# Optimization experiments

Measured on AMD Instinct MI355X. Metric: run time of the kernel, lower is better.

The kernel has to match this reference:

```python
import jax, jax.numpy as jnp
import numpy as np

N_QUBITS = 8
N_CYCLES = 4
N_GATES = 10
MEAS_QUBITS = (3, 7)
BATCH = 16384


def _apply_ry_batched(state, angles, w):
    # angles: [B] per-example RY angle on wire w. state: [B,2,...,2]
    half = angles * 0.5
    c = jnp.cos(half).astype(jnp.complex64)
    s = jnp.sin(half).astype(jnp.complex64)
    U = jnp.stack([jnp.stack([c, -s], -1), jnp.stack([s, c], -1)], -2)  # [B,2,2]
    st = jnp.moveaxis(state, w + 1, -1)
    st = jnp.einsum('bij,b...j->b...i', U, st)
    return jnp.moveaxis(st, -1, w + 1)


def _apply_cnot(state, c, t):
    st = jnp.moveaxis(state, (c + 1, t + 1), (-2, -1))
    st = jnp.concatenate([st[..., 0:1, :], st[..., 1:2, ::-1]], axis=-2)
    return jnp.moveaxis(st, (-2, -1), (c + 1, t + 1))


def _apply_crx(state, theta, c, t):
    # CRX: RX(theta) on target when control=1 (torchquantum convention)
    half = theta * 0.5
    co = jnp.cos(half).astype(jnp.complex64)
    si = (-1j * jnp.sin(half)).astype(jnp.complex64)
    st = jnp.moveaxis(state, (c + 1, t + 1), (-2, -1))
    s1 = st[..., 1, :]
    s1 = jnp.stack([co * s1[..., 0] + si * s1[..., 1],
                    si * s1[..., 0] + co * s1[..., 1]], -1)
    st = jnp.concatenate([st[..., 0:1, :], s1[..., None, :]], axis=-2)
    return jnp.moveaxis(st, (-2, -1), (c + 1, t + 1))


def _expval_z(probs, w):
    axes = tuple(a for a in range(1, N_QUBITS + 1) if a != w + 1)
    m = jnp.sum(probs, axis=axes)  # [B,2]
    return m[:, 0] - m[:, 1]


def _forward(x, crx_theta, w1, b1, w2, b2):
    B = x.shape[0]
    state = jnp.zeros((B, 2 ** N_QUBITS), jnp.complex64).at[:, 0].set(1.0)
    state = state.reshape((B,) + (2,) * N_QUBITS)
    # encoding ansatz: per cycle, RY(x[:,cyc,q]) on each qubit + CNOT ring
    for cyc in range(N_CYCLES):
        for q in range(N_QUBITS):
            state = _apply_ry_batched(state, x[:, cyc, q], q)
        for q in range(N_QUBITS):
            state = _apply_cnot(state, q, (q + 1) % N_QUBITS)
    # trainable CRX layer
    for i in range(N_GATES):
        state = _apply_crx(state, crx_theta[i], i % N_QUBITS, (i + 1) % N_QUBITS)
    probs = jnp.abs(state) ** 2  # real, [B,2,...,2]
    feats = jnp.stack([_expval_z(probs, q) for q in MEAS_QUBITS], -1)  # [B,2]
    h = jnp.tanh(feats @ w1.T + b1)
    return jax.nn.sigmoid(h @ w2.T + b2)  # [B,1]


def setup_inputs() -> dict:
    key = jax.random.key(0)
    ks = jax.random.split(key, 6)
    x = jax.random.normal(ks[0], (BATCH, N_CYCLES, N_QUBITS), jnp.float32)
    crx_theta = jax.random.normal(ks[1], (N_GATES,), jnp.float32) * 0.1
    w1 = jax.random.normal(ks[2], (10, 2), jnp.float32) * (1.0 / np.sqrt(2.0))
    b1 = jnp.zeros((10,), jnp.float32)
    w2 = jax.random.normal(ks[3], (1, 10), jnp.float32) * (1.0 / np.sqrt(10.0))
    b2 = jnp.zeros((1,), jnp.float32)
    return {"x": x, "crx_theta": crx_theta, "w1": w1, "b1": b1, "w2": w2, "b2": b2}


def reference(x, crx_theta, w1, b1, w2, b2):
    return _forward(x, crx_theta, w1, b1, w2, b2)
```

## Files before the change

kernel.cpp:

```cpp
#include <hip/hip_runtime.h>
#include <math.h>


typedef _Float16 h2 __attribute__((ext_vector_type(2)));

#define H2I(v) __builtin_bit_cast(int, (v))
#define I2H(v) __builtin_bit_cast(h2, (v))
#define RLF(v, i) __int_as_float(__builtin_amdgcn_readlane(__float_as_int(v), (i)))
#define RLH(v, i) I2H(__builtin_amdgcn_readlane(H2I(v), (i)))
#define BPH(a, v) I2H(__builtin_amdgcn_ds_bpermute((a), H2I(v)))
#define BPFS(a, v) __int_as_float(__builtin_amdgcn_ds_bpermute((a), __float_as_int(v)))
#define DPPH(v, ctrl) I2H(__builtin_amdgcn_update_dpp(0, H2I(v), (ctrl), 0xf, 0xf, true))
#define DPPF(v, ctrl) __uint_as_float((unsigned)__builtin_amdgcn_update_dpp( \
    0, (int)__float_as_uint(v), (ctrl), 0xf, 0xf, true))
#define NEGH(v) I2H(H2I(v) ^ 0x80008000)
#define SELH(c, a, b) I2H((c) ? H2I(a) : H2I(b))
#define FMH(a, b, c) __builtin_elementwise_fma((a), (b), (c))
#define HONE  I2H(0x3C003C00)
#define HZERO I2H(0)

#define PX1H(v)  DPPH((v), 0xB1)
#define PX2H(v)  DPPH((v), 0x4E)
#define PX4H(v)  DPPH(DPPH((v), 0x141), 0x1B)
#define PX8H(v)  DPPH((v), 0x128)
#define BP16(v)  BPH(a16, (v))
#define BP32(v)  BPH(a32, (v))
#define PX1S(v)  DPPF((v), 0xB1)
#define PX2S(v)  DPPF((v), 0x4E)
#define PX4S(v)  DPPF(DPPF((v), 0x141), 0x1B)
#define PX8S(v)  DPPF((v), 0x128)

__device__ __forceinline__ h2 mkh(float a, float b) {
    h2 r; r.x = (_Float16)a; r.y = (_Float16)b; return r;
}

__global__ __launch_bounds__(256, 8) void vqcnn_wave(
    const float* __restrict__ x,
    const float* __restrict__ crx_theta,
    const float* __restrict__ w1,
    const float* __restrict__ b1,
    const float* __restrict__ w2,
    const float* __restrict__ b2,
    float* __restrict__ out)
{
    const int lane = threadIdx.x & 63;
    const int bA   = blockIdx.x * 8 + (threadIdx.x >> 6) * 2;
    const int bB   = bA + 1;

    float cvA, svA, cvB, svB;
    {
        float aA = 0.f, aB = 0.f;
        if (lane < 32)      { aA = x[bA * 32 + lane]; aB = x[bB * 32 + lane]; }
        else if (lane < 42) { aA = aB = crx_theta[lane - 32]; }
        __sincosf(0.5f * aA, &svA, &cvA);
        __sincosf(0.5f * aB, &svB, &cvB);
    }
    const h2 cvP = mkh(cvA, cvB);
    const h2 svP = mkh(svA, svB);

    const int a16 = (lane ^ 16) << 2;
    const int a32 = (lane ^ 32) << 2;
    const int g0  = lane ^ (lane >> 1);
    const int aE  = g0 << 2;
    const int aO  = (g0 ^ 32) << 2;
    const bool l0r = (lane & 1) != 0;

    h2 vv0, vv1, vv2, vv3;
    {
        float LA = (lane & 32) ? RLF(svA, 3) : RLF(cvA, 3);
        float LB = (lane & 32) ? RLF(svB, 3) : RLF(cvB, 3);
        LA *= (lane & 16) ? RLF(svA, 4) : RLF(cvA, 4);
        LB *= (lane & 16) ? RLF(svB, 4) : RLF(cvB, 4);
        LA *= (lane &  8) ? RLF(svA, 5) : RLF(cvA, 5);
        LB *= (lane &  8) ? RLF(svB, 5) : RLF(cvB, 5);
        LA *= (lane &  4) ? RLF(svA, 6) : RLF(cvA, 6);
        LB *= (lane &  4) ? RLF(svB, 6) : RLF(cvB, 6);
        LA *= (lane &  2) ? RLF(svA, 7) : RLF(cvA, 7);
        LB *= (lane &  2) ? RLF(svB, 7) : RLF(cvB, 7);
        LA *= (lane &  1) ? RLF(svA, 0) : RLF(cvA, 0);
        LB *= (lane &  1) ? RLF(svB, 0) : RLF(cvB, 0);
        const float c1A = RLF(cvA, 1), s1A = RLF(svA, 1);
        const float c2A = RLF(cvA, 2), s2A = RLF(svA, 2);
        const float c1B = RLF(cvB, 1), s1B = RLF(svB, 1);
        const float c2B = RLF(cvB, 2), s2B = RLF(svB, 2);
        vv0 = mkh(LA * c1A * c2A, LB * c1B * c2B);
        vv1 = mkh(LA * c1A * s2A, LB * c1B * s2B);
        vv2 = mkh(LA * s1A * c2A, LB * s1B * c2B);
        vv3 = mkh(LA * s1A * s2A, LB * s1B * s2B);
    }

#define RINGH() {                                                            \
    const h2 z0 = SELH(l0r, vv2, vv0);                                       \
    const h2 z1 = SELH(l0r, vv3, vv1);                                       \
    const h2 z2 = SELH(l0r, vv1, vv3);                                       \
    const h2 z3 = SELH(l0r, vv0, vv2);                                       \
    vv0 = BPH(aE, z0); vv1 = BPH(aO, z1);                                    \
    vv2 = BPH(aE, z2); vv3 = BPH(aO, z3); }
    RINGH()

#define RY_L(ia, mask, EX) {                                                 \
    const h2 c = RLH(cvP, (ia)), s = RLH(svP, (ia));                         \
    const h2 sn = SELH((lane & (mask)) != 0, s, NEGH(s));                    \
    const h2 p0 = EX(vv0), p1 = EX(vv1);                                     \
    const h2 p2 = EX(vv2), p3 = EX(vv3);                                     \
    vv0 = FMH(sn, p0, c * vv0); vv1 = FMH(sn, p1, c * vv1);                  \
    vv2 = FMH(sn, p2, c * vv2); vv3 = FMH(sn, p3, c * vv3); }

#define RY_S1(ia) {                                                          \
    const h2 c = RLH(cvP, (ia)), s = RLH(svP, (ia)), ns = NEGH(s);           \
    const h2 n0 = FMH(ns, vv2, c * vv0), n2 = FMH(s, vv0, c * vv2);          \
    const h2 n1 = FMH(ns, vv3, c * vv1), n3 = FMH(s, vv1, c * vv3);          \
    vv0 = n0; vv1 = n1; vv2 = n2; vv3 = n3; }

#define RY_S0(ia) {                                                          \
    const h2 c = RLH(cvP, (ia)), s = RLH(svP, (ia)), ns = NEGH(s);           \
    const h2 n0 = FMH(ns, vv1, c * vv0), n1 = FMH(s, vv0, c * vv1);          \
    const h2 n2 = FMH(ns, vv3, c * vv2), n3 = FMH(s, vv2, c * vv3);          \
    vv0 = n0; vv1 = n1; vv2 = n2; vv3 = n3; }

    #pragma unroll
    for (int cyc = 1; cyc < 4; ++cyc) {
        const int base = cyc * 8;
        RY_L(base + 0,  1, PX1H)
        RY_S1(base + 1)
        RY_S0(base + 2)
        RY_L(base + 3, 32, BP32)
        RY_L(base + 4, 16, BP16)
        RY_L(base + 5,  8, PX8H)
        RY_L(base + 6,  4, PX4H)
        RY_L(base + 7,  2, PX2H)
        RINGH()
    }

    h2 rr0 = vv0, rr1 = vv1, rr2 = vv2, rr3 = vv3;
    h2 ii0 = HZERO, ii1 = HZERO, ii2 = HZERO, ii3 = HZERO;

#define CRX_G(gi, cmask, EX) {                                               \
    const bool ct = (lane & (cmask)) != 0;                                   \
    const h2 c = SELH(ct, RLH(cvP, 32 + (gi)), HONE);                        \
    const h2 s = SELH(ct, RLH(svP, 32 + (gi)), HZERO);                       \
    const h2 ns = NEGH(s);                                                   \
    const h2 pr0 = EX(rr0), pi0 = EX(ii0);                                   \
    const h2 pr1 = EX(rr1), pi1 = EX(ii1);                                   \
    const h2 pr2 = EX(rr2), pi2 = EX(ii2);                                   \
    const h2 pr3 = EX(rr3), pi3 = EX(ii3);                                   \
    rr0 = FMH(s, pi0, c * rr0); ii0 = FMH(ns, pr0, c * ii0);                 \
    rr1 = FMH(s, pi1, c * rr1); ii1 = FMH(ns, pr1, c * ii1);                 \
    rr2 = FMH(s, pi2, c * rr2); ii2 = FMH(ns, pr2, c * ii2);                 \
    rr3 = FMH(s, pi3, c * rr3); ii3 = FMH(ns, pr3, c * ii3); }

#define CRX_SLOT1(gi) {                                                      \
    const bool ct = (lane & 1) != 0;                                         \
    const h2 c = SELH(ct, RLH(cvP, 32 + (gi)), HONE);                        \
    const h2 s = SELH(ct, RLH(svP, 32 + (gi)), HZERO);                       \
    const h2 ns = NEGH(s);                                                   \
    const h2 nr0 = FMH(s, ii2, c * rr0), ni0 = FMH(ns, rr2, c * ii0);        \
    const h2 nr2 = FMH(s, ii0, c * rr2), ni2 = FMH(ns, rr0, c * ii2);        \
    const h2 nr1 = FMH(s, ii3, c * rr1), ni1 = FMH(ns, rr3, c * ii1);        \
    const h2 nr3 = FMH(s, ii1, c * rr3), ni3 = FMH(ns, rr1, c * ii3);        \
    rr0 = nr0; ii0 = ni0; rr1 = nr1; ii1 = ni1;                              \
    rr2 = nr2; ii2 = ni2; rr3 = nr3; ii3 = ni3; }

#define CRX_SLOT0(gi) {                                                      \
    const h2 c = RLH(cvP, 32 + (gi)), s = RLH(svP, 32 + (gi)), ns = NEGH(s); \
    const h2 nr2 = FMH(s, ii3, c * rr2), ni2 = FMH(ns, rr3, c * ii2);        \
    const h2 nr3 = FMH(s, ii2, c * rr3), ni3 = FMH(ns, rr2, c * ii3);        \
    rr2 = nr2; ii2 = ni2; rr3 = nr3; ii3 = ni3; }

    CRX_SLOT1(0)
    CRX_SLOT0(1)
    {
        const h2 c = RLH(cvP, 34), s = RLH(svP, 34), ns = NEGH(s);
        const h2 pr1 = BP32(rr1), pi1 = BP32(ii1);
        const h2 pr3 = BP32(rr3), pi3 = BP32(ii3);
        rr1 = FMH(s, pi1, c * rr1); ii1 = FMH(ns, pr1, c * ii1);
        rr3 = FMH(s, pi3, c * rr3); ii3 = FMH(ns, pr3, c * ii3);
    }
    CRX_G(3, 32, BP16)
    CRX_G(4, 16, PX8H)
    CRX_G(5,  8, PX4H)
    CRX_G(6,  4, PX2H)
    CRX_G(7,  2, PX1H)
    CRX_SLOT1(8)
    CRX_SLOT0(9)

    const h2 pp0 = FMH(rr0, rr0, ii0 * ii0);
    const h2 pp1 = FMH(rr1, rr1, ii1 * ii1);
    const h2 pp2 = FMH(rr2, rr2, ii2 * ii2);
    const h2 pp3 = FMH(rr3, rr3, ii3 * ii3);
    const h2 ap  = (pp0 + pp1) + (pp2 + pp3);
    const float aA = (float)ap.x, aB = (float)ap.y;
    float z3A = (lane & 32) ? -aA : aA, z3B = (lane & 32) ? -aB : aB;
    float z7A = (lane &  2) ? -aA : aA, z7B = (lane &  2) ? -aB : aB;
    z3A += PX1S(z3A); z3B += PX1S(z3B); z7A += PX1S(z7A); z7B += PX1S(z7B);
    z3A += PX2S(z3A); z3B += PX2S(z3B); z7A += PX2S(z7A); z7B += PX2S(z7B);
    z3A += PX4S(z3A); z3B += PX4S(z3B); z7A += PX4S(z7A); z7B += PX4S(z7B);
    z3A += PX8S(z3A); z3B += PX8S(z3B); z7A += PX8S(z7A); z7B += PX8S(z7B);
    z3A += BPFS(a16, z3A); z3B += BPFS(a16, z3B);
    z7A += BPFS(a16, z7A); z7B += BPFS(a16, z7B);
    z3A += BPFS(a32, z3A); z3B += BPFS(a32, z3B);
    z7A += BPFS(a32, z7A); z7B += BPFS(a32, z7B);

    float wa = 0.f, wb = 0.f, bb = 0.f, wc = 0.f;
    if (lane < 10) {
        wa = w1[2 * lane];
        wb = w1[2 * lane + 1];
        bb = b1[lane];
        wc = w2[lane];
    }
    const float zA = fmaf(wa, z3A, fmaf(wb, z7A, bb));
    const float zB = fmaf(wa, z3B, fmaf(wb, z7B, bb));
    const float eA = __expf(2.0f * zA), eB = __expf(2.0f * zB);
    const float hA = 1.0f - 2.0f * __builtin_amdgcn_rcpf(eA + 1.0f);
    const float hB = 1.0f - 2.0f * __builtin_amdgcn_rcpf(eB + 1.0f);
    float accA = wc * hA, accB = wc * hB;
    accA += PX1S(accA); accB += PX1S(accB);
    accA += PX2S(accA); accB += PX2S(accB);
    accA += PX4S(accA); accB += PX4S(accB);
    accA += PX8S(accA); accB += PX8S(accB);
    if (lane == 0) {
        const float bias = b2[0];
        out[bA] = __builtin_amdgcn_rcpf(1.0f + __expf(-(accA + bias)));
        out[bB] = __builtin_amdgcn_rcpf(1.0f + __expf(-(accB + bias)));
    }
}

extern "C" void kernel_launch(void* const* d_in, const int* in_sizes, int n_in,
                              void* d_out, int out_size, void* d_ws, size_t ws_size,
                              hipStream_t stream) {
    const float* x         = (const float*)d_in[0];
    const float* crx_theta = (const float*)d_in[1];
    const float* w1        = (const float*)d_in[2];
    const float* b1        = (const float*)d_in[3];
    const float* w2        = (const float*)d_in[4];
    const float* b2        = (const float*)d_in[5];
    float* out = (float*)d_out;

    const int B = in_sizes[0] / 32;
    vqcnn_wave<<<B / 8, 256, 0, stream>>>(x, crx_theta, w1, b1, w2, b2, out);
}
```

Before: 75.62 us.

## Process four batch elements per wave with interleaved gate streams

Each wave now simulates four examples, held as two packed-half state sets interleaved gate by gate, instead of two. The interleaving supplies independent instruction chains to hide DPP and bpermute latency, and it amortizes the lane-index setup and readlane overhead. The final reduction is restructured to share the common butterfly stages before the z3/z7 sign split, and outputs are written as a single float4. The cost is roughly double the register pressure, which launch bounds allow by dropping to 4 blocks, and half as many blocks in the grid.

After: 76.26 us. Within noise of the previous version (+0.8%).

```diff
diff --git a/kernel.cpp b/kernel.cpp
--- a/kernel.cpp
+++ b/kernel.cpp
@@ -34,7 +34,7 @@
     h2 r; r.x = (_Float16)a; r.y = (_Float16)b; return r;
 }
 
-__global__ __launch_bounds__(256, 8) void vqcnn_wave(
+__global__ __launch_bounds__(256, 4) void vqcnn_wave(
     const float* __restrict__ x,
     const float* __restrict__ crx_theta,
     const float* __restrict__ w1,
@@ -44,19 +44,24 @@
     float* __restrict__ out)
 {
     const int lane = threadIdx.x & 63;
-    const int bA   = blockIdx.x * 8 + (threadIdx.x >> 6) * 2;
-    const int bB   = bA + 1;
-
-    float cvA, svA, cvB, svB;
+    const int b0   = blockIdx.x * 16 + (threadIdx.x >> 6) * 4;
+
+    float cvA, svA, cvB, svB, cvC, svC, cvD, svD;
     {
-        float aA = 0.f, aB = 0.f;
-        if (lane < 32)      { aA = x[bA * 32 + lane]; aB = x[bB * 32 + lane]; }
-        else if (lane < 42) { aA = aB = crx_theta[lane - 32]; }
+        float aA = 0.f, aB = 0.f, aC = 0.f, aD = 0.f;
+        if (lane < 32) {
+            aA = x[(b0 + 0) * 32 + lane]; aB = x[(b0 + 1) * 32 + lane];
+            aC = x[(b0 + 2) * 32 + lane]; aD = x[(b0 + 3) * 32 + lane];
+        } else if (lane < 42) {
+            aA = aB = aC = aD = crx_theta[lane - 32];
+        }
         __sincosf(0.5f * aA, &svA, &cvA);
         __sincosf(0.5f * aB, &svB, &cvB);
+        __sincosf(0.5f * aC, &svC, &cvC);
+        __sincosf(0.5f * aD, &svD, &cvD);
     }
-    const h2 cvP = mkh(cvA, cvB);
-    const h2 svP = mkh(svA, svB);
+    const h2 cvP = mkh(cvA, cvB), svP = mkh(svA, svB);
+    const h2 cvQ = mkh(cvC, cvD), svQ = mkh(svC, svD);
 
     const int a16 = (lane ^ 16) << 2;
     const int a32 = (lane ^ 32) << 2;
@@ -65,141 +70,185 @@
     const int aO  = (g0 ^ 32) << 2;
     const bool l0r = (lane & 1) != 0;
 
-    h2 vv0, vv1, vv2, vv3;
-    {
-        float LA = (lane & 32) ? RLF(svA, 3) : RLF(cvA, 3);
-        float LB = (lane & 32) ? RLF(svB, 3) : RLF(cvB, 3);
-        LA *= (lane & 16) ? RLF(svA, 4) : RLF(cvA, 4);
-        LB *= (lane & 16) ? RLF(svB, 4) : RLF(cvB, 4);
-        LA *= (lane &  8) ? RLF(svA, 5) : RLF(cvA, 5);
-        LB *= (lane &  8) ? RLF(svB, 5) : RLF(cvB, 5);
-        LA *= (lane &  4) ? RLF(svA, 6) : RLF(cvA, 6);
-        LB *= (lane &  4) ? RLF(svB, 6) : RLF(cvB, 6);
-        LA *= (lane &  2) ? RLF(svA, 7) : RLF(cvA, 7);
-        LB *= (lane &  2) ? RLF(svB, 7) : RLF(cvB, 7);
-        LA *= (lane &  1) ? RLF(svA, 0) : RLF(cvA, 0);
-        LB *= (lane &  1) ? RLF(svB, 0) : RLF(cvB, 0);
-        const float c1A = RLF(cvA, 1), s1A = RLF(svA, 1);
-        const float c2A = RLF(cvA, 2), s2A = RLF(svA, 2);
-        const float c1B = RLF(cvB, 1), s1B = RLF(svB, 1);
-        const float c2B = RLF(cvB, 2), s2B = RLF(svB, 2);
-        vv0 = mkh(LA * c1A * c2A, LB * c1B * c2B);
-        vv1 = mkh(LA * c1A * s2A, LB * c1B * s2B);
-        vv2 = mkh(LA * s1A * c2A, LB * s1B * c2B);
-        vv3 = mkh(LA * s1A * s2A, LB * s1B * s2B);
-    }
-
-#define RINGH() {                                                            \
-    const h2 z0 = SELH(l0r, vv2, vv0);                                       \
-    const h2 z1 = SELH(l0r, vv3, vv1);                                       \
-    const h2 z2 = SELH(l0r, vv1, vv3);                                       \
-    const h2 z3 = SELH(l0r, vv0, vv2);                                       \
-    vv0 = BPH(aE, z0); vv1 = BPH(aO, z1);                                    \
-    vv2 = BPH(aE, z2); vv3 = BPH(aO, z3); }
-    RINGH()
-
-#define RY_L(ia, mask, EX) {                                                 \
-    const h2 c = RLH(cvP, (ia)), s = RLH(svP, (ia));                         \
-    const h2 sn = SELH((lane & (mask)) != 0, s, NEGH(s));                    \
-    const h2 p0 = EX(vv0), p1 = EX(vv1);                                     \
-    const h2 p2 = EX(vv2), p3 = EX(vv3);                                     \
-    vv0 = FMH(sn, p0, c * vv0); vv1 = FMH(sn, p1, c * vv1);                  \
-    vv2 = FMH(sn, p2, c * vv2); vv3 = FMH(sn, p3, c * vv3); }
-
-#define RY_S1(ia) {                                                          \
-    const h2 c = RLH(cvP, (ia)), s = RLH(svP, (ia)), ns = NEGH(s);           \
-    const h2 n0 = FMH(ns, vv2, c * vv0), n2 = FMH(s, vv0, c * vv2);          \
-    const h2 n1 = FMH(ns, vv3, c * vv1), n3 = FMH(s, vv1, c * vv3);          \
-    vv0 = n0; vv1 = n1; vv2 = n2; vv3 = n3; }
-
-#define RY_S0(ia) {                                                          \
-    const h2 c = RLH(cvP, (ia)), s = RLH(svP, (ia)), ns = NEGH(s);           \
-    const h2 n0 = FMH(ns, vv1, c * vv0), n1 = FMH(s, vv0, c * vv1);          \
-    const h2 n2 = FMH(ns, vv3, c * vv2), n3 = FMH(s, vv2, c * vv3);          \
-    vv0 = n0; vv1 = n1; vv2 = n2; vv3 = n3; }
+    const int sg1  = (lane &  1) ? 0 : 0x80008000;
+    const int sg2  = (lane &  2) ? 0 : 0x80008000;
+    const int sg4  = (lane &  4) ? 0 : 0x80008000;
+    const int sg8  = (lane &  8) ? 0 : 0x80008000;
+    const int sg16 = (lane & 16) ? 0 : 0x80008000;
+    const int sg32 = (lane & 32) ? 0 : 0x80008000;
+
+#define INIT0(V0, V1, V2, V3, CVa, SVa, CVb, SVb) {                          \
+    float _LA = (lane & 32) ? RLF(SVa, 3) : RLF(CVa, 3);       \
+    float _LB = (lane & 32) ? RLF(SVb, 3) : RLF(CVb, 3);                     \
+    _LA *= (lane & 16) ? RLF(SVa, 4) : RLF(CVa, 4);            \
+    _LB *= (lane & 16) ? RLF(SVb, 4) : RLF(CVb, 4);                          \
+    _LA *= (lane &  8) ? RLF(SVa, 5) : RLF(CVa, 5);            \
+    _LB *= (lane &  8) ? RLF(SVb, 5) : RLF(CVb, 5);                          \
+    _LA *= (lane &  4) ? RLF(SVa, 6) : RLF(CVa, 6);            \
+    _LB *= (lane &  4) ? RLF(SVb, 6) : RLF(CVb, 6);                          \
+    _LA *= (lane &  2) ? RLF(SVa, 7) : RLF(CVa, 7);            \
+    _LB *= (lane &  2) ? RLF(SVb, 7) : RLF(CVb, 7);                          \
+    _LA *= (lane &  1) ? RLF(SVa, 0) : RLF(CVa, 0);            \
+    _LB *= (lane &  1) ? RLF(SVb, 0) : RLF(CVb, 0);                          \
+    const float _c1a = RLF(CVa, 1), _s1a = RLF(SVa, 1);        \
+    const float _c2a = RLF(CVa, 2), _s2a = RLF(SVa, 2);        \
+    const float _c1b = RLF(CVb, 1), _s1b = RLF(SVb, 1);                      \
+    const float _c2b = RLF(CVb, 2), _s2b = RLF(SVb, 2);                      \
+    V0 = mkh(_LA * _c1a * _c2a, _LB * _c1b * _c2b);                          \
+    V1 = mkh(_LA * _c1a * _s2a, _LB * _c1b * _s2b);                          \
+    V2 = mkh(_LA * _s1a * _c2a, _LB * _s1b * _c2b);                          \
+    V3 = mkh(_LA * _s1a * _s2a, _LB * _s1b * _s2b); }
+
+    h2 vP0, vP1, vP2, vP3, vQ0, vQ1, vQ2, vQ3;
+    INIT0(vP0, vP1, vP2, vP3, cvA, svA, cvB, svB)
+    INIT0(vQ0, vQ1, vQ2, vQ3, cvC, svC, cvD, svD)
+
+#define RING1(V0, V1, V2, V3) {                                              \
+    const h2 _z0 = SELH(l0r, V2, V0);                                        \
+    const h2 _z1 = SELH(l0r, V3, V1);                                        \
+    const h2 _z2 = SELH(l0r, V1, V3);                                        \
+    const h2 _z3 = SELH(l0r, V0, V2);                                        \
+    V0 = BPH(aE, _z0); V1 = BPH(aO, _z1);                                    \
+    V2 = BPH(aE, _z2); V3 = BPH(aO, _z3); }
+
+    RING1(vP0, vP1, vP2, vP3)
+    RING1(vQ0, vQ1, vQ2, vQ3)
+
+#define RY_L1(V0, V1, V2, V3, CT, ST, ia, sgm, EX) {                         \
+    const h2 _c = RLH(CT, (ia)), _s = RLH(ST, (ia));                         \
+    const h2 _sn = I2H(H2I(_s) ^ (sgm));                                     \
+    const h2 _p0 = EX(V0), _p1 = EX(V1);                                     \
+    const h2 _p2 = EX(V2), _p3 = EX(V3);                                     \
+    V0 = FMH(_sn, _p0, _c * V0); V1 = FMH(_sn, _p1, _c * V1);                \
+    V2 = FMH(_sn, _p2, _c * V2); V3 = FMH(_sn, _p3, _c * V3); }
+
+#define RY_S1a(V0, V1, V2, V3, CT, ST, ia) {                                 \
+    const h2 _c = RLH(CT, (ia)), _s = RLH(ST, (ia)), _ns = NEGH(_s);         \
+    const h2 _n0 = FMH(_ns, V2, _c * V0), _n2 = FMH(_s, V0, _c * V2);        \
+    const h2 _n1 = FMH(_ns, V3, _c * V1), _n3 = FMH(_s, V1, _c * V3);        \
+    V0 = _n0; V1 = _n1; V2 = _n2; V3 = _n3; }
+
+#define RY_S0a(V0, V1, V2, V3, CT, ST, ia) {                                 \
+    const h2 _c = RLH(CT, (ia)), _s = RLH(ST, (ia)), _ns = NEGH(_s);         \
+    const h2 _n0 = FMH(_ns, V1, _c * V0), _n1 = FMH(_s, V0, _c * V1);        \
+    const h2 _n2 = FMH(_ns, V3, _c * V2), _n3 = FMH(_s, V2, _c * V3);        \
+    V0 = _n0; V1 = _n1; V2 = _n2; V3 = _n3; }
 
     #pragma unroll
     for (int cyc = 1; cyc < 4; ++cyc) {
         const int base = cyc * 8;
-        RY_L(base + 0,  1, PX1H)
-        RY_S1(base + 1)
-        RY_S0(base + 2)
-        RY_L(base + 3, 32, BP32)
-        RY_L(base + 4, 16, BP16)
-        RY_L(base + 5,  8, PX8H)
-        RY_L(base + 6,  4, PX4H)
-        RY_L(base + 7,  2, PX2H)
-        RINGH()
+        RY_L1(vP0, vP1, vP2, vP3, cvP, svP, base + 0, sg1, PX1H)
+        RY_L1(vQ0, vQ1, vQ2, vQ3, cvQ, svQ, base + 0, sg1, PX1H)
+        RY_S1a(vP0, vP1, vP2, vP3, cvP, svP, base + 1)
+        RY_S1a(vQ0, vQ1, vQ2, vQ3, cvQ, svQ, base + 1)
+        RY_S0a(vP0, vP1, vP2, vP3, cvP, svP, base + 2)
+        RY_S0a(vQ0, vQ1, vQ2, vQ3, cvQ, svQ, base + 2)
+        RY_L1(vP0, vP1, vP2, vP3, cvP, svP, base + 3, sg32, BP32)
+        RY_L1(vQ0, vQ1, vQ2, vQ3, cvQ, svQ, base + 3, sg32, BP32)
+        RY_L1(vP0, vP1, vP2, vP3, cvP, svP, base + 4, sg16, BP16)
+        RY_L1(vQ0, vQ1, vQ2, vQ3, cvQ, svQ, base + 4, sg16, BP16)
+        RY_L1(vP0, vP1, vP2, vP3, cvP, svP, base + 5, sg8, PX8H)
+        RY_L1(vQ0, vQ1, vQ2, vQ3, cvQ, svQ, base + 5, sg8, PX8H)
+        RY_L1(vP0, vP1, vP2, vP3, cvP, svP, base + 6, sg4, PX4H)
+        RY_L1(vQ0, vQ1, vQ2, vQ3, cvQ, svQ, base + 6, sg4, PX4H)
+        RY_L1(vP0, vP1, vP2, vP3, cvP, svP, base + 7, sg2, PX2H)
+        RY_L1(vQ0, vQ1, vQ2, vQ3, cvQ, svQ, base + 7, sg2, PX2H)
+        RING1(vP0, vP1, vP2, vP3)
+        RING1(vQ0, vQ1, vQ2, vQ3)
     }
 
-    h2 rr0 = vv0, rr1 = vv1, rr2 = vv2, rr3 = vv3;
-    h2 ii0 = HZERO, ii1 = HZERO, ii2 = HZERO, ii3 = HZERO;
-
-#define CRX_G(gi, cmask, EX) {                                               \
-    const bool ct = (lane & (cmask)) != 0;                                   \
-    const h2 c = SELH(ct, RLH(cvP, 32 + (gi)), HONE);                        \
-    const h2 s = SELH(ct, RLH(svP, 32 + (gi)), HZERO);                       \
-    const h2 ns = NEGH(s);                                                   \
-    const h2 pr0 = EX(rr0), pi0 = EX(ii0);                                   \
-    const h2 pr1 = EX(rr1), pi1 = EX(ii1);                                   \
-    const h2 pr2 = EX(rr2), pi2 = EX(ii2);                                   \
-    const h2 pr3 = EX(rr3), pi3 = EX(ii3);                                   \
-    rr0 = FMH(s, pi0, c * rr0); ii0 = FMH(ns, pr0, c * ii0);                 \
-    rr1 = FMH(s, pi1, c * rr1); ii1 = FMH(ns, pr1, c * ii1);                 \
-    rr2 = FMH(s, pi2, c * rr2); ii2 = FMH(ns, pr2, c * ii2);                 \
-    rr3 = FMH(s, pi3, c * rr3); ii3 = FMH(ns, pr3, c * ii3); }
-
-#define CRX_SLOT1(gi) {                                                      \
-    const bool ct = (lane & 1) != 0;                                         \
-    const h2 c = SELH(ct, RLH(cvP, 32 + (gi)), HONE);                        \
-    const h2 s = SELH(ct, RLH(svP, 32 + (gi)), HZERO);                       \
-    const h2 ns = NEGH(s);                                                   \
-    const h2 nr0 = FMH(s, ii2, c * rr0), ni0 = FMH(ns, rr2, c * ii0);        \
-    const h2 nr2 = FMH(s, ii0, c * rr2), ni2 = FMH(ns, rr0, c * ii2);        \
-    const h2 nr1 = FMH(s, ii3, c * rr1), ni1 = FMH(ns, rr3, c * ii1);        \
-    const h2 nr3 = FMH(s, ii1, c * rr3), ni3 = FMH(ns, rr1, c * ii3);        \
-    rr0 = nr0; ii0 = ni0; rr1 = nr1; ii1 = ni1;                              \
-    rr2 = nr2; ii2 = ni2; rr3 = nr3; ii3 = ni3; }
-
-#define CRX_SLOT0(gi) {                                                      \
-    const h2 c = RLH(cvP, 32 + (gi)), s = RLH(svP, 32 + (gi)), ns = NEGH(s); \
-    const h2 nr2 = FMH(s, ii3, c * rr2), ni2 = FMH(ns, rr3, c * ii2);        \
-    const h2 nr3 = FMH(s, ii2, c * rr3), ni3 = FMH(ns, rr2, c * ii3);        \
-    rr2 = nr2; ii2 = ni2; rr3 = nr3; ii3 = ni3; }
-
-    CRX_SLOT1(0)
-    CRX_SLOT0(1)
-    {
-        const h2 c = RLH(cvP, 34), s = RLH(svP, 34), ns = NEGH(s);
-        const h2 pr1 = BP32(rr1), pi1 = BP32(ii1);
-        const h2 pr3 = BP32(rr3), pi3 = BP32(ii3);
-        rr1 = FMH(s, pi1, c * rr1); ii1 = FMH(ns, pr1, c * ii1);
-        rr3 = FMH(s, pi3, c * rr3); ii3 = FMH(ns, pr3, c * ii3);
-    }
-    CRX_G(3, 32, BP16)
-    CRX_G(4, 16, PX8H)
-    CRX_G(5,  8, PX4H)
-    CRX_G(6,  4, PX2H)
-    CRX_G(7,  2, PX1H)
-    CRX_SLOT1(8)
-    CRX_SLOT0(9)
-
-    const h2 pp0 = FMH(rr0, rr0, ii0 * ii0);
-    const h2 pp1 = FMH(rr1, rr1, ii1 * ii1);
-    const h2 pp2 = FMH(rr2, rr2, ii2 * ii2);
-    const h2 pp3 = FMH(rr3, rr3, ii3 * ii3);
-    const h2 ap  = (pp0 + pp1) + (pp2 + pp3);
-    const float aA = (float)ap.x, aB = (float)ap.y;
-    float z3A = (lane & 32) ? -aA : aA, z3B = (lane & 32) ? -aB : aB;
-    float z7A = (lane &  2) ? -aA : aA, z7B = (lane &  2) ? -aB : aB;
-    z3A += PX1S(z3A); z3B += PX1S(z3B); z7A += PX1S(z7A); z7B += PX1S(z7B);
-    z3A += PX2S(z3A); z3B += PX2S(z3B); z7A += PX2S(z7A); z7B += PX2S(z7B);
-    z3A += PX4S(z3A); z3B += PX4S(z3B); z7A += PX4S(z7A); z7B += PX4S(z7B);
-    z3A += PX8S(z3A); z3B += PX8S(z3B); z7A += PX8S(z7A); z7B += PX8S(z7B);
-    z3A += BPFS(a16, z3A); z3B += BPFS(a16, z3B);
-    z7A += BPFS(a16, z7A); z7B += BPFS(a16, z7B);
-    z3A += BPFS(a32, z3A); z3B += BPFS(a32, z3B);
-    z7A += BPFS(a32, z7A); z7B += BPFS(a32, z7B);
+    h2 rP0 = vP0, rP1 = vP1, rP2 = vP2, rP3 = vP3;
+    h2 iP0 = HZERO, iP1 = HZERO, iP2 = HZERO, iP3 = HZERO;
+    h2 rQ0 = vQ0, rQ1 = vQ1, rQ2 = vQ2, rQ3 = vQ3;
+    h2 iQ0 = HZERO, iQ1 = HZERO, iQ2 = HZERO, iQ3 = HZERO;
+
+#define CRX_Ga(R0, R1, R2, R3, I0, I1, I2, I3, CT, ST, gi, cmask, EX) {      \
+    const bool _ct = (lane & (cmask)) != 0;                                  \
+    const h2 _c = SELH(_ct, RLH(CT, 32 + (gi)), HONE);                       \
+    const h2 _s = SELH(_ct, RLH(ST, 32 + (gi)), HZERO);                      \
+    const h2 _ns = NEGH(_s);                                                 \
+    const h2 _pr0 = EX(R0), _pi0 = EX(I0);                                   \
+    const h2 _pr1 = EX(R1), _pi1 = EX(I1);                                   \
+    const h2 _pr2 = EX(R2), _pi2 = EX(I2);                                   \
+    const h2 _pr3 = EX(R3), _pi3 = EX(I3);                                   \
+    R0 = FMH(_s, _pi0, _c * R0); I0 = FMH(_ns, _pr0, _c * I0);               \
+    R1 = FMH(_s, _pi1, _c * R1); I1 = FMH(_ns, _pr1, _c * I1);               \
+    R2 = FMH(_s, _pi2, _c * R2); I2 = FMH(_ns, _pr2, _c * I2);               \
+    R3 = FMH(_s, _pi3, _c * R3); I3 = FMH(_ns, _pr3, _c * I3); }
+
+#define CRX_SLOT1a(R0, R1, R2, R3, I0, I1, I2, I3, CT, ST, gi) {             \
+    const bool _ct = (lane & 1) != 0;                                        \
+    const h2 _c = SELH(_ct, RLH(CT, 32 + (gi)), HONE);                       \
+    const h2 _s = SELH(_ct, RLH(ST, 32 + (gi)), HZERO);                      \
+    const h2 _ns = NEGH(_s);                                                 \
+    const h2 _nr0 = FMH(_s, I2, _c * R0), _ni0 = FMH(_ns, R2, _c * I0);      \
+    const h2 _nr2 = FMH(_s, I0, _c * R2), _ni2 = FMH(_ns, R0, _c * I2);      \
+    const h2 _nr1 = FMH(_s, I3, _c * R1), _ni1 = FMH(_ns, R3, _c * I1);      \
+    const h2 _nr3 = FMH(_s, I1, _c * R3), _ni3 = FMH(_ns, R1, _c * I3);      \
+    R0 = _nr0; I0 = _ni0; R1 = _nr1; I1 = _ni1;                              \
+    R2 = _nr2; I2 = _ni2; R3 = _nr3; I3 = _ni3; }
+
+#define CRX_SLOT0a(R2, R3, I2, I3, CT, ST, gi) {                             \
+    const h2 _c = RLH(CT, 32 + (gi)), _s = RLH(ST, 32 + (gi));               \
+    const h2 _ns = NEGH(_s);                                                 \
+    const h2 _nr2 = FMH(_s, I3, _c * R2), _ni2 = FMH(_ns, R3, _c * I2);      \
+    const h2 _nr3 = FMH(_s, I2, _c * R3), _ni3 = FMH(_ns, R2, _c * I3);      \
+    R2 = _nr2; I2 = _ni2; R3 = _nr3; I3 = _ni3; }
+
+#define CRX_I2(R1, R3, I1, I3, CT, ST) {                                     \
+    const h2 _c = RLH(CT, 34), _s = RLH(ST, 34), _ns = NEGH(_s);             \
+    const h2 _pr1 = BP32(R1), _pi1 = BP32(I1);                               \
+    const h2 _pr3 = BP32(R3), _pi3 = BP32(I3);                               \
+    R1 = FMH(_s, _pi1, _c * R1); I1 = FMH(_ns, _pr1, _c * I1);               \
+    R3 = FMH(_s, _pi3, _c * R3); I3 = FMH(_ns, _pr3, _c * I3); }
+
+    CRX_SLOT1a(rP0, rP1, rP2, rP3, iP0, iP1, iP2, iP3, cvP, svP, 0)
+    CRX_SLOT1a(rQ0, rQ1, rQ2, rQ3, iQ0, iQ1, iQ2, iQ3, cvQ, svQ, 0)
+    CRX_SLOT0a(rP2, rP3, iP2, iP3, cvP, svP, 1)
+    CRX_SLOT0a(rQ2, rQ3, iQ2, iQ3, cvQ, svQ, 1)
+    CRX_I2(rP1, rP3, iP1, iP3, cvP, svP)
+    CRX_I2(rQ1, rQ3, iQ1, iQ3, cvQ, svQ)
+    CRX_Ga(rP0, rP1, rP2, rP3, iP0, iP1, iP2, iP3, cvP, svP, 3, 32, BP16)
+    CRX_Ga(rQ0, rQ1, rQ2, rQ3, iQ0, iQ1, iQ2, iQ3, cvQ, svQ, 3, 32, BP16)
+    CRX_Ga(rP0, rP1, rP2, rP3, iP0, iP1, iP2, iP3, cvP, svP, 4, 16, PX8H)
+    CRX_Ga(rQ0, rQ1, rQ2, rQ3, iQ0, iQ1, iQ2, iQ3, cvQ, svQ, 4, 16, PX8H)
+    CRX_Ga(rP0, rP1, rP2, rP3, iP0, iP1, iP2, iP3, cvP, svP, 5, 8, PX4H)
+    CRX_Ga(rQ0, rQ1, rQ2, rQ3, iQ0, iQ1, iQ2, iQ3, cvQ, svQ, 5, 8, PX4H)
+    CRX_Ga(rP0, rP1, rP2, rP3, iP0, iP1, iP2, iP3, cvP, svP, 6, 4, PX2H)
+    CRX_Ga(rQ0, rQ1, rQ2, rQ3, iQ0, iQ1, iQ2, iQ3, cvQ, svQ, 6, 4, PX2H)
+    CRX_Ga(rP0, rP1, rP2, rP3, iP0, iP1, iP2, iP3, cvP, svP, 7, 2, PX1H)
+    CRX_Ga(rQ0, rQ1, rQ2, rQ3, iQ0, iQ1, iQ2, iQ3, cvQ, svQ, 7, 2, PX1H)
+    CRX_SLOT1a(rP0, rP1, rP2, rP3, iP0, iP1, iP2, iP3, cvP, svP, 8)
+    CRX_SLOT1a(rQ0, rQ1, rQ2, rQ3, iQ0, iQ1, iQ2, iQ3, cvQ, svQ, 8)
+    CRX_SLOT0a(rP2, rP3, iP2, iP3, cvP, svP, 9)
+    CRX_SLOT0a(rQ2, rQ3, iQ2, iQ3, cvQ, svQ, 9)
+
+    const h2 pP0 = FMH(rP0, rP0, iP0 * iP0);
+    const h2 pP1 = FMH(rP1, rP1, iP1 * iP1);
+    const h2 pP2 = FMH(rP2, rP2, iP2 * iP2);
+    const h2 pP3 = FMH(rP3, rP3, iP3 * iP3);
+    const h2 apP = (pP0 + pP1) + (pP2 + pP3);
+    const h2 pQ0 = FMH(rQ0, rQ0, iQ0 * iQ0);
+    const h2 pQ1 = FMH(rQ1, rQ1, iQ1 * iQ1);
+    const h2 pQ2 = FMH(rQ2, rQ2, iQ2 * iQ2);
+    const h2 pQ3 = FMH(rQ3, rQ3, iQ3 * iQ3);
+    const h2 apQ = (pQ0 + pQ1) + (pQ2 + pQ3);
+    float aAf = (float)apP.x, aBf = (float)apP.y;
+    float aCf = (float)apQ.x, aDf = (float)apQ.y;
+
+#define RED4(v) { v += PX1S(v); v += PX4S(v); v += PX8S(v); v += BPFS(a16, v); }
+    RED4(aAf) RED4(aBf) RED4(aCf) RED4(aDf)
+
+#define ZPAIR(af, Z3, Z7)                                                    \
+    float Z3 = (lane & 32) ? -(af) : (af);         \
+    Z3 += BPFS(a32, Z3); Z3 += PX2S(Z3);                                     \
+    float Z7 = (lane & 2) ? -(af) : (af);          \
+    Z7 += PX2S(Z7); Z7 += BPFS(a32, Z7);
+
+    ZPAIR(aAf, z3A, z7A)
+    ZPAIR(aBf, z3B, z7B)
+    ZPAIR(aCf, z3C, z7C)
+    ZPAIR(aDf, z3D, z7D)
 
     float wa = 0.f, wb = 0.f, bb = 0.f, wc = 0.f;
     if (lane < 10) {
@@ -210,18 +259,28 @@
     }
     const float zA = fmaf(wa, z3A, fmaf(wb, z7A, bb));
     const float zB = fmaf(wa, z3B, fmaf(wb, z7B, bb));
+    const float zC = fmaf(wa, z3C, fmaf(wb, z7C, bb));
+    const float zD = fmaf(wa, z3D, fmaf(wb, z7D, bb));
     const float eA = __expf(2.0f * zA), eB = __expf(2.0f * zB);
+    const float eC = __expf(2.0f * zC), eD = __expf(2.0f * zD);
     const float hA = 1.0f - 2.0f * __builtin_amdgcn_rcpf(eA + 1.0f);
     const float hB = 1.0f - 2.0f * __builtin_amdgcn_rcpf(eB + 1.0f);
+    const float hC = 1.0f - 2.0f * __builtin_amdgcn_rcpf(eC + 1.0f);
+    const float hD = 1.0f - 2.0f * __builtin_amdgcn_rcpf(eD + 1.0f);
     float accA = wc * hA, accB = wc * hB;
-    accA += PX1S(accA); accB += PX1S(accB);
-    accA += PX2S(accA); accB += PX2S(accB);
-    accA += PX4S(accA); accB += PX4S(accB);
-    accA += PX8S(accA); accB += PX8S(accB);
+    float accC = wc * hC, accD = wc * hD;
+    accA += PX1S(accA); accB += PX1S(accB); accC += PX1S(accC); accD += PX1S(accD);
+    accA += PX2S(accA); accB += PX2S(accB); accC += PX2S(accC); accD += PX2S(accD);
+    accA += PX4S(accA); accB += PX4S(accB); accC += PX4S(accC); accD += PX4S(accD);
+    accA += PX8S(accA); accB += PX8S(accB); accC += PX8S(accC); accD += PX8S(accD);
     if (lane == 0) {
         const float bias = b2[0];
-        out[bA] = __builtin_amdgcn_rcpf(1.0f + __expf(-(accA + bias)));
-        out[bB] = __builtin_amdgcn_rcpf(1.0f + __expf(-(accB + bias)));
+        float4 o;
+        o.x = __builtin_amdgcn_rcpf(1.0f + __expf(-(accA + bias)));
+        o.y = __builtin_amdgcn_rcpf(1.0f + __expf(-(accB + bias)));
+        o.z = __builtin_amdgcn_rcpf(1.0f + __expf(-(accC + bias)));
+        o.w = __builtin_amdgcn_rcpf(1.0f + __expf(-(accD + bias)));
+        *reinterpret_cast<float4*>(out + b0) = o;
     }
 }
 
@@ -237,5 +296,5 @@
     float* out = (float*)d_out;
 
     const int B = in_sizes[0] / 32;
-    vqcnn_wave<<<B / 8, 256, 0, stream>>>(x, crx_theta, w1, b1, w2, b2, out);
+    vqcnn_wave<<<B / 16, 256, 0, stream>>>(x, crx_theta, w1, b1, w2, b2, out);
 }
```
